# Performance work log

Measured on AMD Instinct MI355X. Metric: run time of the kernel, lower is better.

The kernel has to match this reference:

```python
import jax, jax.numpy as jnp
import numpy as np

EPS = 1e-12  # torch F.normalize eps


def setup_inputs() -> dict:
    key = jax.random.key(0)
    k1, k2, k3 = jax.random.split(key, 3)
    N, C, H, W = 64, 512, 30, 30
    K = 64
    x = jax.random.normal(k1, (N, C, H, W), dtype=jnp.float32)
    conv_w = jax.random.normal(k2, (K, C), dtype=jnp.float32) * 0.02
    centroids = jax.random.uniform(k3, (K, C), dtype=jnp.float32)
    return {"x": x, "conv_w": conv_w, "centroids": centroids}


def reference(x, conv_w, centroids):
    N, C, H, W = x.shape
    K = conv_w.shape[0]
    # descriptor-wise L2 normalization over channel dim (torch F.normalize, p=2, dim=1)
    norm = jnp.sqrt(jnp.sum(x * x, axis=1, keepdims=True))
    x = x / jnp.maximum(norm, EPS)
    xf = x.reshape(N, C, H * W)  # [N, C, P]
    # 1x1 conv (no bias) -> logits [N, K, P]; softmax over clusters K
    logits = jnp.einsum("ncp,kc->nkp", xf, conv_w)
    a = jax.nn.softmax(logits, axis=1)  # [N, K, P]
    # vlad[n,k,c] = sum_p a[n,k,p] * (x[n,c,p] - centroids[k,c])
    #            = (a @ x^T)[n,k,c] - centroids[k,c] * sum_p a[n,k,p]
    vlad = jnp.einsum("nkp,ncp->nkc", a, xf) - a.sum(axis=-1)[:, :, None] * centroids[None]
    return vlad
```

## Files before the change

kernel.cpp:

```cpp
#include <hip/hip_runtime.h>

typedef __attribute__((ext_vector_type(8))) __bf16 bf16x8;
typedef __attribute__((ext_vector_type(4))) __bf16 bf16x4;
typedef __attribute__((ext_vector_type(4))) float f32x4;

#define LGKM_BAR() do { asm volatile("s_waitcnt lgkmcnt(0)" ::: "memory"); \
                        __builtin_amdgcn_s_barrier(); } while (0)

namespace {
constexpr int N_ = 64, C_ = 512, P_ = 900, K_ = 64;
constexpr int PP = 960;
constexpr size_t TOT_X = (size_t)N_ * C_ * P_;
constexpr size_t AT_BYTES = (size_t)N_ * K_ * PP * 2;
constexpr size_t ASUM_OFF = AT_BYTES;
constexpr size_t WBR_OFF  = ASUM_OFF + (size_t)N_ * K_ * 4;
}

__global__ __launch_bounds__(256) void k_prep_w(const float* __restrict__ w,
                                                __bf16* __restrict__ wbr,
                                                float* __restrict__ asum) {
  const int T = blockIdx.x * 256 + threadIdx.x;
  const int k = T >> 6, oct = T & 63;
  const float4 a = *reinterpret_cast<const float4*>(w + (size_t)k * C_ + oct * 8);
  const float4 b = *reinterpret_cast<const float4*>(w + (size_t)k * C_ + oct * 8 + 4);
  bf16x8 o = { (__bf16)a.x, (__bf16)a.y, (__bf16)a.z, (__bf16)a.w,
               (__bf16)b.x, (__bf16)b.y, (__bf16)b.z, (__bf16)b.w };
  *reinterpret_cast<bf16x8*>(wbr + ((size_t)oct * K_ + k) * 8) = o;
  asum[T] = 0.f;
}

__global__ __launch_bounds__(512) void k_phase1(const float* __restrict__ x,
                                                const __bf16* __restrict__ wbr,
                                                __bf16* __restrict__ at,
                                                float* __restrict__ asum) {
  __shared__ bf16x8 Wl[4096];
  const int n   = blockIdx.y;
  const int tid = threadIdx.x;
  const int w   = tid >> 6, l = tid & 63;
  const int l15 = l & 15,  lh = l >> 4;
  const int p   = blockIdx.x * 128 + w * 16 + l15;
  const int pc  = p < P_ ? p : P_ - 1;
  const float* xp = x + (size_t)n * C_ * P_ + (size_t)lh * 8 * P_ + pc;

  bf16x8 tmp[8];
  #pragma unroll
  for (int it = 0; it < 8; ++it)
    tmp[it] = *reinterpret_cast<const bf16x8*>(wbr + (size_t)(it * 512 + tid) * 8);

  float g[6][8];
  #pragma unroll
  for (int b = 0; b < 6; ++b)
    #pragma unroll
    for (int j = 0; j < 8; ++j)
      g[b][j] = xp[(size_t)(b * 32 + j) * P_];

  #pragma unroll
  for (int it = 0; it < 8; ++it)
    Wl[it * 512 + tid] = tmp[it];
  LGKM_BAR();

  f32x4 acc[4] = {};
  float sq = 0.f;
  #pragma unroll
  for (int s = 0; s < 16; ++s) {
    bf16x8 b;
    #pragma unroll
    for (int j = 0; j < 8; ++j) {
      const float v = g[s % 6][j];
      sq = fmaf(v, v, sq); b[j] = (__bf16)v;
    }
    if (s + 6 < 16) {
      #pragma unroll
      for (int j = 0; j < 8; ++j)
        g[s % 6][j] = xp[(size_t)((s + 6) * 32 + j) * P_];
    }
    #pragma unroll
    for (int m = 0; m < 4; ++m) {
      bf16x8 a = Wl[(s * 4 + lh) * 64 + 16 * m + l15];
      acc[m] = __builtin_amdgcn_mfma_f32_16x16x32_bf16(a, b, acc[m], 0, 0, 0);
    }
  }

  sq += __shfl_xor(sq, 16, 64);
  sq += __shfl_xor(sq, 32, 64);
  const float invn = 1.f / fmaxf(sqrtf(sq), 1e-12f);
  const bool  valid = p < P_;

  float ps = 0.f;
  #pragma unroll
  for (int m = 0; m < 4; ++m)
    #pragma unroll
    for (int r = 0; r < 4; ++r) {
      acc[m][r] = __expf(acc[m][r] * invn);
      ps += acc[m][r];
    }
  ps += __shfl_xor(ps, 16, 64);
  ps += __shfl_xor(ps, 32, 64);
  const float invs = 1.f / ps;
  const float sc   = invs * invn;

  if (p < PP) {
    #pragma unroll
    for (int m = 0; m < 4; ++m)
      #pragma unroll
      for (int r = 0; r < 4; ++r) {
        const int k = 16 * m + lh * 4 + r;
        at[((size_t)n * K_ + k) * PP + p] =
            valid ? (__bf16)(acc[m][r] * sc) : (__bf16)0.f;
      }
  }
  #pragma unroll
  for (int m = 0; m < 4; ++m)
    #pragma unroll
    for (int r = 0; r < 4; ++r) {
      float v = valid ? acc[m][r] * invs : 0.f;
      v += __shfl_xor(v, 1, 64); v += __shfl_xor(v, 2, 64);
      v += __shfl_xor(v, 4, 64); v += __shfl_xor(v, 8, 64);
      if (l15 == 0)
        unsafeAtomicAdd(asum + n * K_ + 16 * m + lh * 4 + r, v);
    }
}

__global__ __launch_bounds__(256) void k_phase2(const float* __restrict__ x,
                                                const __bf16* __restrict__ at,
                                                const float* __restrict__ asum,
                                                const float* __restrict__ cent,
                                                float* __restrict__ out) {
  __shared__ __bf16 Al[2][64][40];
  __shared__ __bf16 Xl[2][64][40];
  const int n   = blockIdx.y;
  const int c0  = blockIdx.x * 64;
  const int tid = threadIdx.x;
  const int w   = tid >> 6, l = tid & 63;
  const int l15 = l & 15,  lh = l >> 4;

  const int ak  = tid >> 2, ach = tid & 3;
  const int xc  = tid >> 3, xch = tid & 7;
  const size_t abase  = ((size_t)n * K_ + ak) * PP + ach * 8;
  const size_t xbase0 = ((size_t)n * C_ + c0 + xc) * P_ + xch * 4;
  const size_t xbase1 = ((size_t)n * C_ + c0 + xc + 32) * P_ + xch * 4;

  f32x4 acc[4] = {};
  bf16x8 na; float4 v0, v1;

  auto LOAD = [&](int s) {
    na = *reinterpret_cast<const bf16x8*>(at + abase + s * 32);
    size_t o0 = xbase0 + s * 32; if (o0 > TOT_X - 4) o0 = TOT_X - 4;
    size_t o1 = xbase1 + s * 32; if (o1 > TOT_X - 4) o1 = TOT_X - 4;
    v0 = *reinterpret_cast<const float4*>(x + o0);
    v1 = *reinterpret_cast<const float4*>(x + o1);
  };
  auto STORE = [&](int b) {
    *reinterpret_cast<bf16x8*>(&Al[b][ak][ach * 8]) = na;
    bf16x4 p0 = { (__bf16)v0.x, (__bf16)v0.y, (__bf16)v0.z, (__bf16)v0.w };
    bf16x4 p1 = { (__bf16)v1.x, (__bf16)v1.y, (__bf16)v1.z, (__bf16)v1.w };
    *reinterpret_cast<bf16x4*>(&Xl[b][xc][xch * 4])      = p0;
    *reinterpret_cast<bf16x4*>(&Xl[b][xc + 32][xch * 4]) = p1;
  };

  LOAD(0); STORE(0);
  LGKM_BAR();

  #pragma unroll 2
  for (int s = 0; s < 29; ++s) {
    if (s < 28) LOAD(s + 1);
    bf16x8 b = *reinterpret_cast<const bf16x8*>(&Xl[s & 1][16 * w + l15][lh * 8]);
    #pragma unroll
    for (int m = 0; m < 4; ++m) {
      bf16x8 a = *reinterpret_cast<const bf16x8*>(&Al[s & 1][16 * m + l15][lh * 8]);
      acc[m] = __builtin_amdgcn_mfma_f32_16x16x32_bf16(a, b, acc[m], 0, 0, 0);
    }
    if (s < 28) STORE((s + 1) & 1);
    LGKM_BAR();
  }

  const int c = c0 + 16 * w + l15;
  #pragma unroll
  for (int m = 0; m < 4; ++m) {
    #pragma unroll
    for (int r = 0; r < 4; ++r) {
      const int k = 16 * m + lh * 4 + r;
      out[((size_t)n * K_ + k) * C_ + c] =
          acc[m][r] - asum[n * K_ + k] * cent[(size_t)k * C_ + c];
    }
  }
}

extern "C" void kernel_launch(void* const* d_in, const int* in_sizes, int n_in,
                              void* d_out, int out_size, void* d_ws, size_t ws_size,
                              hipStream_t stream) {
  const float* x    = (const float*)d_in[0];
  const float* w    = (const float*)d_in[1];
  const float* cent = (const float*)d_in[2];
  float* out = (float*)d_out;
  char* wsb  = (char*)d_ws;
  __bf16* at   = (__bf16*)wsb;
  float*  asum = (float*)(wsb + ASUM_OFF);
  __bf16* wbr  = (__bf16*)(wsb + WBR_OFF);

  k_prep_w<<<dim3(16), dim3(256), 0, stream>>>(w, wbr, asum);
  k_phase1<<<dim3(8, 64), dim3(512), 0, stream>>>(x, wbr, at, asum);
  k_phase2<<<dim3(8, 64), dim3(256), 0, stream>>>(x, at, asum, cent, out);
}
```

Measured before the change: 69.82 us.

## Stage phase-1 x tiles through LDS with float4 loads and double buffering

Phase 1 now uses 256-thread blocks covering 64 pixels each (15x64 grid). Previously each lane read x directly with scalar strided loads into registers. Now the block loads coalesced float4 rows into a double-buffered bf16 LDS tile and accumulates per-pixel squared norms through LDS atomics. This should improve global load efficiency and spread work over more blocks. In exchange it adds a barrier per step, strided LDS reads to build the MFMA operand, and a 64 KB weight copy into LDS for every block.

```diff
diff --git a/kernel.cpp b/kernel.cpp
--- a/kernel.cpp
+++ b/kernel.cpp
@@ -29,61 +29,78 @@
   asum[T] = 0.f;
 }
 
-__global__ __launch_bounds__(512) void k_phase1(const float* __restrict__ x,
+__global__ __launch_bounds__(256) void k_phase1(const float* __restrict__ x,
                                                 const __bf16* __restrict__ wbr,
                                                 __bf16* __restrict__ at,
                                                 float* __restrict__ asum) {
   __shared__ bf16x8 Wl[4096];
+  __shared__ __bf16 Xl[2][32][66];
+  __shared__ float ssq_l[64];
   const int n   = blockIdx.y;
+  const int p0  = blockIdx.x * 64;
   const int tid = threadIdx.x;
   const int w   = tid >> 6, l = tid & 63;
   const int l15 = l & 15,  lh = l >> 4;
-  const int p   = blockIdx.x * 128 + w * 16 + l15;
-  const int pc  = p < P_ ? p : P_ - 1;
-  const float* xp = x + (size_t)n * C_ * P_ + (size_t)lh * 8 * P_ + pc;
-
-  bf16x8 tmp[8];
-  #pragma unroll
-  for (int it = 0; it < 8; ++it)
-    tmp[it] = *reinterpret_cast<const bf16x8*>(wbr + (size_t)(it * 512 + tid) * 8);
-
-  float g[6][8];
-  #pragma unroll
-  for (int b = 0; b < 6; ++b)
-    #pragma unroll
-    for (int j = 0; j < 8; ++j)
-      g[b][j] = xp[(size_t)(b * 32 + j) * P_];
-
-  #pragma unroll
-  for (int it = 0; it < 8; ++it)
-    Wl[it * 512 + tid] = tmp[it];
+  const int p   = p0 + w * 16 + l15;
+
+  bf16x8 tmp[16];
+  #pragma unroll
+  for (int it = 0; it < 16; ++it)
+    tmp[it] = *reinterpret_cast<const bf16x8*>(wbr + (size_t)(it * 256 + tid) * 8);
+  #pragma unroll
+  for (int it = 0; it < 16; ++it)
+    Wl[it * 256 + tid] = tmp[it];
+  if (tid < 64) ssq_l[tid] = 0.f;
+
+  const int sc = tid >> 4, pq = (tid & 15) * 4;
+  const bool pvalid = (p0 + pq) < P_;
+  const size_t xs = (size_t)n * C_ * P_ + p0 + pq;
+  float f[8];
+  float sq[4] = {0.f, 0.f, 0.f, 0.f};
+
+  auto LOAD = [&](int s) {
+    if (pvalid) {
+      const float4 v0 = *reinterpret_cast<const float4*>(x + xs + (size_t)(s * 32 + sc) * P_);
+      const float4 v1 = *reinterpret_cast<const float4*>(x + xs + (size_t)(s * 32 + sc + 16) * P_);
+      f[0]=v0.x; f[1]=v0.y; f[2]=v0.z; f[3]=v0.w;
+      f[4]=v1.x; f[5]=v1.y; f[6]=v1.z; f[7]=v1.w;
+    } else {
+      #pragma unroll
+      for (int j = 0; j < 8; ++j) f[j] = 0.f;
+    }
+  };
+  auto STORE = [&](int b) {
+    #pragma unroll
+    for (int j = 0; j < 8; ++j) sq[j & 3] = fmaf(f[j], f[j], sq[j & 3]);
+    bf16x4 a0 = { (__bf16)f[0], (__bf16)f[1], (__bf16)f[2], (__bf16)f[3] };
+    bf16x4 a1 = { (__bf16)f[4], (__bf16)f[5], (__bf16)f[6], (__bf16)f[7] };
+    *reinterpret_cast<bf16x4*>(&Xl[b][sc][pq])      = a0;
+    *reinterpret_cast<bf16x4*>(&Xl[b][sc + 16][pq]) = a1;
+  };
+
+  LOAD(0); STORE(0);
   LGKM_BAR();
 
   f32x4 acc[4] = {};
-  float sq = 0.f;
   #pragma unroll
   for (int s = 0; s < 16; ++s) {
+    if (s < 15) LOAD(s + 1);
     bf16x8 b;
     #pragma unroll
-    for (int j = 0; j < 8; ++j) {
-      const float v = g[s % 6][j];
-      sq = fmaf(v, v, sq); b[j] = (__bf16)v;
-    }
-    if (s + 6 < 16) {
-      #pragma unroll
-      for (int j = 0; j < 8; ++j)
-        g[s % 6][j] = xp[(size_t)((s + 6) * 32 + j) * P_];
-    }
+    for (int j = 0; j < 8; ++j) b[j] = Xl[s & 1][lh * 8 + j][w * 16 + l15];
     #pragma unroll
     for (int m = 0; m < 4; ++m) {
       bf16x8 a = Wl[(s * 4 + lh) * 64 + 16 * m + l15];
       acc[m] = __builtin_amdgcn_mfma_f32_16x16x32_bf16(a, b, acc[m], 0, 0, 0);
     }
+    if (s < 15) { STORE((s + 1) & 1); LGKM_BAR(); }
   }
 
-  sq += __shfl_xor(sq, 16, 64);
-  sq += __shfl_xor(sq, 32, 64);
-  const float invn = 1.f / fmaxf(sqrtf(sq), 1e-12f);
+  #pragma unroll
+  for (int i = 0; i < 4; ++i) atomicAdd(&ssq_l[pq + i], sq[i]);
+  __syncthreads();
+
+  const float invn = 1.f / fmaxf(sqrtf(ssq_l[w * 16 + l15]), 1e-12f);
   const bool  valid = p < P_;
 
   float ps = 0.f;
@@ -97,18 +114,16 @@
   ps += __shfl_xor(ps, 16, 64);
   ps += __shfl_xor(ps, 32, 64);
   const float invs = 1.f / ps;
-  const float sc   = invs * invn;
-
-  if (p < PP) {
-    #pragma unroll
-    for (int m = 0; m < 4; ++m)
-      #pragma unroll
-      for (int r = 0; r < 4; ++r) {
-        const int k = 16 * m + lh * 4 + r;
-        at[((size_t)n * K_ + k) * PP + p] =
-            valid ? (__bf16)(acc[m][r] * sc) : (__bf16)0.f;
-      }
-  }
+  const float sc2  = invs * invn;
+
+  #pragma unroll
+  for (int m = 0; m < 4; ++m)
+    #pragma unroll
+    for (int r = 0; r < 4; ++r) {
+      const int k = 16 * m + lh * 4 + r;
+      at[((size_t)n * K_ + k) * PP + p] =
+          valid ? (__bf16)(acc[m][r] * sc2) : (__bf16)0.f;
+    }
   #pragma unroll
   for (int m = 0; m < 4; ++m)
     #pragma unroll
@@ -199,6 +214,6 @@
   __bf16* wbr  = (__bf16*)(wsb + WBR_OFF);
 
   k_prep_w<<<dim3(16), dim3(256), 0, stream>>>(w, wbr, asum);
-  k_phase1<<<dim3(8, 64), dim3(512), 0, stream>>>(x, wbr, at, asum);
+  k_phase1<<<dim3(15, 64), dim3(256), 0, stream>>>(x, wbr, at, asum);
   k_phase2<<<dim3(8, 64), dim3(256), 0, stream>>>(x, at, asum, cent, out);
 }
```

Result: slower. 83.58 us (+19.7%).

## Stage x through LDS with coalesced float4 loads in phase1, 256 pixels per block

Applied to the files above, without the earlier changes.

Phase1 previously had each lane gather scalar strided x values straight from global memory. It now loads coalesced float4 rows into a double-buffered bf16 LDS tile and accumulates per-pixel squared norms via LDS atomics. Each block covers 256 pixels, with each wave computing two 16-pixel MFMA tiles, so W fragments are reused across both tiles. The grid halves and a launch_bounds occupancy hint is added, in exchange for more LDS use, a barrier per step and padding work on the last block.

```diff
diff --git a/kernel.cpp b/kernel.cpp
--- a/kernel.cpp
+++ b/kernel.cpp
@@ -1,4 +1,5 @@
 #include <hip/hip_runtime.h>
+#include <stdint.h>
 
 typedef __attribute__((ext_vector_type(8))) __bf16 bf16x8;
 typedef __attribute__((ext_vector_type(4))) __bf16 bf16x4;
@@ -10,10 +11,19 @@
 namespace {
 constexpr int N_ = 64, C_ = 512, P_ = 900, K_ = 64;
 constexpr int PP = 960;
+constexpr int PB = 256;
+constexpr int SROW = 266;
 constexpr size_t TOT_X = (size_t)N_ * C_ * P_;
 constexpr size_t AT_BYTES = (size_t)N_ * K_ * PP * 2;
 constexpr size_t ASUM_OFF = AT_BYTES;
 constexpr size_t WBR_OFF  = ASUM_OFF + (size_t)N_ * K_ * 4;
+}
+
+__device__ inline uint32_t pk2(float a, float b) {
+  __bf16 x = (__bf16)a, y = (__bf16)b;
+  uint16_t xb = *reinterpret_cast<uint16_t*>(&x);
+  uint16_t yb = *reinterpret_cast<uint16_t*>(&y);
+  return ((uint32_t)yb << 16) | xb;
 }
 
 __global__ __launch_bounds__(256) void k_prep_w(const float* __restrict__ w,
@@ -29,91 +39,139 @@
   asum[T] = 0.f;
 }
 
-__global__ __launch_bounds__(512) void k_phase1(const float* __restrict__ x,
-                                                const __bf16* __restrict__ wbr,
-                                                __bf16* __restrict__ at,
-                                                float* __restrict__ asum) {
+__global__ __launch_bounds__(512, 2) void k_phase1(const float* __restrict__ x,
+                                                   const __bf16* __restrict__ wbr,
+                                                   __bf16* __restrict__ at,
+                                                   float* __restrict__ asum) {
+  __shared__ __bf16 Xl[2][32][SROW];
   __shared__ bf16x8 Wl[4096];
+  __shared__ float ssq_l[PB];
   const int n   = blockIdx.y;
+  const int p0  = blockIdx.x * PB;
   const int tid = threadIdx.x;
   const int w   = tid >> 6, l = tid & 63;
   const int l15 = l & 15,  lh = l >> 4;
-  const int p   = blockIdx.x * 128 + w * 16 + l15;
-  const int pc  = p < P_ ? p : P_ - 1;
-  const float* xp = x + (size_t)n * C_ * P_ + (size_t)lh * 8 * P_ + pc;
-
-  bf16x8 tmp[8];
+
+  const int sc = tid >> 4;
+  const int pq = (tid & 15) * 16;
+  const float* xrow = x + (size_t)n * C_ * P_ + p0 + pq;
+
+  bf16x8 tw[8];
   #pragma unroll
   for (int it = 0; it < 8; ++it)
-    tmp[it] = *reinterpret_cast<const bf16x8*>(wbr + (size_t)(it * 512 + tid) * 8);
-
-  float g[6][8];
-  #pragma unroll
-  for (int b = 0; b < 6; ++b)
-    #pragma unroll
-    for (int j = 0; j < 8; ++j)
-      g[b][j] = xp[(size_t)(b * 32 + j) * P_];
-
-  #pragma unroll
-  for (int it = 0; it < 8; ++it)
-    Wl[it * 512 + tid] = tmp[it];
+    tw[it] = *reinterpret_cast<const bf16x8*>(wbr + (size_t)(it * 512 + tid) * 8);
+
+  float4 f[2][4];
+  auto LOAD = [&](int s, int slot) {
+    #pragma unroll
+    for (int i = 0; i < 4; ++i) {
+      const int gp = p0 + pq + i * 4;
+      if (gp <= P_ - 4)
+        f[slot][i] = *reinterpret_cast<const float4*>(
+            xrow + (size_t)(s * 32 + sc) * P_ + i * 4);
+      else
+        f[slot][i] = make_float4(0.f, 0.f, 0.f, 0.f);
+    }
+  };
+
+  float sq[16];
+  #pragma unroll
+  for (int j = 0; j < 16; ++j) sq[j] = 0.f;
+
+  auto STORE = [&](int slot, int b) {
+    #pragma unroll
+    for (int i = 0; i < 4; ++i) {
+      const float4 v = f[slot][i];
+      sq[i*4+0] = fmaf(v.x, v.x, sq[i*4+0]);
+      sq[i*4+1] = fmaf(v.y, v.y, sq[i*4+1]);
+      sq[i*4+2] = fmaf(v.z, v.z, sq[i*4+2]);
+      sq[i*4+3] = fmaf(v.w, v.w, sq[i*4+3]);
+      uint32_t* d = reinterpret_cast<uint32_t*>(&Xl[b][sc][pq + i * 4]);
+      d[0] = pk2(v.x, v.y);
+      d[1] = pk2(v.z, v.w);
+    }
+  };
+
+  LOAD(0, 0); LOAD(1, 1);
+  #pragma unroll
+  for (int it = 0; it < 8; ++it) Wl[it * 512 + tid] = tw[it];
+  if (tid < PB) ssq_l[tid] = 0.f;
+  STORE(0, 0);
   LGKM_BAR();
 
-  f32x4 acc[4] = {};
-  float sq = 0.f;
+  f32x4 acc[2][4] = {};
   #pragma unroll
   for (int s = 0; s < 16; ++s) {
-    bf16x8 b;
-    #pragma unroll
-    for (int j = 0; j < 8; ++j) {
-      const float v = g[s % 6][j];
-      sq = fmaf(v, v, sq); b[j] = (__bf16)v;
-    }
-    if (s + 6 < 16) {
+    if (s + 2 < 16) LOAD(s + 2, s & 1);
+    bf16x8 a[4];
+    #pragma unroll
+    for (int m = 0; m < 4; ++m)
+      a[m] = Wl[(s * 4 + lh) * 64 + 16 * m + l15];
+    #pragma unroll
+    for (int t = 0; t < 2; ++t) {
+      bf16x8 bb;
       #pragma unroll
       for (int j = 0; j < 8; ++j)
-        g[s % 6][j] = xp[(size_t)((s + 6) * 32 + j) * P_];
-    }
-    #pragma unroll
-    for (int m = 0; m < 4; ++m) {
-      bf16x8 a = Wl[(s * 4 + lh) * 64 + 16 * m + l15];
-      acc[m] = __builtin_amdgcn_mfma_f32_16x16x32_bf16(a, b, acc[m], 0, 0, 0);
-    }
-  }
-
-  sq += __shfl_xor(sq, 16, 64);
-  sq += __shfl_xor(sq, 32, 64);
-  const float invn = 1.f / fmaxf(sqrtf(sq), 1e-12f);
-  const bool  valid = p < P_;
-
-  float ps = 0.f;
+        bb[j] = Xl[s & 1][lh * 8 + j][w * 32 + t * 16 + l15];
+      #pragma unroll
+      for (int m = 0; m < 4; ++m)
+        acc[t][m] = __builtin_amdgcn_mfma_f32_16x16x32_bf16(a[m], bb, acc[t][m], 0, 0, 0);
+    }
+    if (s < 15) { STORE((s + 1) & 1, (s + 1) & 1); LGKM_BAR(); }
+  }
+
+  #pragma unroll
+  for (int j = 0; j < 16; ++j) atomicAdd(&ssq_l[pq + j], sq[j]);
+  __syncthreads();
+
+  float invn[2], invs[2];
+  bool  val[2];
+  int   pp[2];
+  #pragma unroll
+  for (int t = 0; t < 2; ++t) {
+    pp[t]   = p0 + w * 32 + t * 16 + l15;
+    invn[t] = 1.f / fmaxf(sqrtf(ssq_l[w * 32 + t * 16 + l15]), 1e-12f);
+    val[t]  = pp[t] < P_;
+  }
+  float ps[2] = {0.f, 0.f};
+  #pragma unroll
+  for (int t = 0; t < 2; ++t)
+    #pragma unroll
+    for (int m = 0; m < 4; ++m)
+      #pragma unroll
+      for (int r = 0; r < 4; ++r) {
+        acc[t][m][r] = __expf(acc[t][m][r] * invn[t]);
+        ps[t] += acc[t][m][r];
+      }
+  #pragma unroll
+  for (int t = 0; t < 2; ++t) {
+    ps[t] += __shfl_xor(ps[t], 16, 64);
+    ps[t] += __shfl_xor(ps[t], 32, 64);
+    invs[t] = 1.f / ps[t];
+  }
+
+  #pragma unroll
+  for (int t = 0; t < 2; ++t) {
+    if (pp[t] < PP) {
+      const float sc2 = invs[t] * invn[t];
+      #pragma unroll
+      for (int m = 0; m < 4; ++m)
+        #pragma unroll
+        for (int r = 0; r < 4; ++r) {
+          const int k = 16 * m + lh * 4 + r;
+          at[((size_t)n * K_ + k) * PP + pp[t]] =
+              val[t] ? (__bf16)(acc[t][m][r] * sc2) : (__bf16)0.f;
+        }
+    }
+  }
   #pragma unroll
   for (int m = 0; m < 4; ++m)
     #pragma unroll
     for (int r = 0; r < 4; ++r) {
-      acc[m][r] = __expf(acc[m][r] * invn);
-      ps += acc[m][r];
-    }
-  ps += __shfl_xor(ps, 16, 64);
-  ps += __shfl_xor(ps, 32, 64);
-  const float invs = 1.f / ps;
-  const float sc   = invs * invn;
-
-  if (p < PP) {
-    #pragma unroll
-    for (int m = 0; m < 4; ++m)
-      #pragma unroll
-      for (int r = 0; r < 4; ++r) {
-        const int k = 16 * m + lh * 4 + r;
-        at[((size_t)n * K_ + k) * PP + p] =
-            valid ? (__bf16)(acc[m][r] * sc) : (__bf16)0.f;
-      }
-  }
-  #pragma unroll
-  for (int m = 0; m < 4; ++m)
-    #pragma unroll
-    for (int r = 0; r < 4; ++r) {
-      float v = valid ? acc[m][r] * invs : 0.f;
+      float v = 0.f;
+      #pragma unroll
+      for (int t = 0; t < 2; ++t)
+        v += val[t] ? acc[t][m][r] * invs[t] : 0.f;
       v += __shfl_xor(v, 1, 64); v += __shfl_xor(v, 2, 64);
       v += __shfl_xor(v, 4, 64); v += __shfl_xor(v, 8, 64);
       if (l15 == 0)
@@ -199,6 +257,6 @@
   __bf16* wbr  = (__bf16*)(wsb + WBR_OFF);
 
   k_prep_w<<<dim3(16), dim3(256), 0, stream>>>(w, wbr, asum);
-  k_phase1<<<dim3(8, 64), dim3(512), 0, stream>>>(x, wbr, at, asum);
+  k_phase1<<<dim3(4, 64), dim3(512), 0, stream>>>(x, wbr, at, asum);
   k_phase2<<<dim3(8, 64), dim3(256), 0, stream>>>(x, at, asum, cent, out);
 }
```

Result: slower. 99.03 us (+41.8%).

## Split phase1 into channel-quarter logit partials plus separate softmax kernel

Applied to the files above, without the earlier changes.

Phase1 now has each block stage a 128-channel quarter of one image through LDS with coalesced float4 loads. It writes partial bf16 logits and partial squared norms per quarter. A new softmax kernel sums the four partials, applies normalization, softmax and the cluster sums, then writes the assignment matrix. This replaces strided per-pixel column loads with coalesced ones, at the cost of an extra launch, extra workspace traffic for the partials, and bf16 rounding of the partial logits.

```diff
diff --git a/kernel.cpp b/kernel.cpp
--- a/kernel.cpp
+++ b/kernel.cpp
@@ -1,4 +1,5 @@
 #include <hip/hip_runtime.h>
+#include <stdint.h>
 
 typedef __attribute__((ext_vector_type(8))) __bf16 bf16x8;
 typedef __attribute__((ext_vector_type(4))) __bf16 bf16x4;
@@ -10,10 +11,13 @@
 namespace {
 constexpr int N_ = 64, C_ = 512, P_ = 900, K_ = 64;
 constexpr int PP = 960;
+constexpr int XROW = 962;
 constexpr size_t TOT_X = (size_t)N_ * C_ * P_;
 constexpr size_t AT_BYTES = (size_t)N_ * K_ * PP * 2;
 constexpr size_t ASUM_OFF = AT_BYTES;
 constexpr size_t WBR_OFF  = ASUM_OFF + (size_t)N_ * K_ * 4;
+constexpr size_t SSQ_OFF  = WBR_OFF + (size_t)K_ * C_ * 2;
+constexpr size_t LQ_OFF   = SSQ_OFF + (size_t)4 * N_ * PP * 4;
 }
 
 __global__ __launch_bounds__(256) void k_prep_w(const float* __restrict__ w,
@@ -31,94 +35,171 @@
 
 __global__ __launch_bounds__(512) void k_phase1(const float* __restrict__ x,
                                                 const __bf16* __restrict__ wbr,
-                                                __bf16* __restrict__ at,
-                                                float* __restrict__ asum) {
-  __shared__ bf16x8 Wl[4096];
-  const int n   = blockIdx.y;
+                                                __bf16* __restrict__ Lq,
+                                                float* __restrict__ ssqq) {
+  __shared__ __bf16 Xa[2][32][XROW];
+  __shared__ bf16x8 Wl[1024];
+  const int bid = blockIdx.x;
+  const int n = bid >> 2, q = bid & 3;
   const int tid = threadIdx.x;
-  const int w   = tid >> 6, l = tid & 63;
-  const int l15 = l & 15,  lh = l >> 4;
-  const int p   = blockIdx.x * 128 + w * 16 + l15;
-  const int pc  = p < P_ ? p : P_ - 1;
-  const float* xp = x + (size_t)n * C_ * P_ + (size_t)lh * 8 * P_ + pc;
-
-  bf16x8 tmp[8];
-  #pragma unroll
-  for (int it = 0; it < 8; ++it)
-    tmp[it] = *reinterpret_cast<const bf16x8*>(wbr + (size_t)(it * 512 + tid) * 8);
-
-  float g[6][8];
-  #pragma unroll
-  for (int b = 0; b < 6; ++b)
-    #pragma unroll
-    for (int j = 0; j < 8; ++j)
-      g[b][j] = xp[(size_t)(b * 32 + j) * P_];
-
-  #pragma unroll
-  for (int it = 0; it < 8; ++it)
-    Wl[it * 512 + tid] = tmp[it];
+  const int w = tid >> 6, l = tid & 63;
+  const int l15 = l & 15, lh = l >> 4;
+  const int wk = w >> 2, wp = w & 3;
+
+  {
+    const bf16x8* wq = reinterpret_cast<const bf16x8*>(wbr) + (size_t)q * 1024;
+    bf16x8 t0 = wq[tid], t1 = wq[512 + tid];
+    Wl[tid] = t0; Wl[512 + tid] = t1;
+  }
+  for (int idx = tid; idx < 2 * 32 * 62; idx += 512) {
+    const int b = idx / 1984, r = idx - b * 1984;
+    Xa[b][r / 62][900 + r % 62] = (__bf16)0.f;
+  }
+
+  const float* xbase = x + ((size_t)n * C_ + q * 128) * P_;
+  float4 ring[15];
+  const bool stg = tid < 480;
+
+  auto LOADS = [&](int s) {
+    if (stg) {
+      #pragma unroll
+      for (int i = 0; i < 15; ++i)
+        ring[i] = *reinterpret_cast<const float4*>(
+            xbase + (size_t)s * 28800 + (size_t)(tid + i * 480) * 4);
+    }
+  };
+  auto STORES = [&](int buf) {
+    if (stg) {
+      #pragma unroll
+      for (int i = 0; i < 15; ++i) {
+        const int fo = tid + i * 480;
+        const int c = fo / 225, pq4 = (fo - c * 225) * 4;
+        const float4 v = ring[i];
+        bf16x4 o = { (__bf16)v.x, (__bf16)v.y, (__bf16)v.z, (__bf16)v.w };
+        *reinterpret_cast<bf16x4*>(&Xa[buf][c][pq4]) = o;
+      }
+    }
+  };
+
+  LOADS(0); STORES(0);
   LGKM_BAR();
 
-  f32x4 acc[4] = {};
-  float sq = 0.f;
-  #pragma unroll
-  for (int s = 0; s < 16; ++s) {
-    bf16x8 b;
-    #pragma unroll
-    for (int j = 0; j < 8; ++j) {
-      const float v = g[s % 6][j];
-      sq = fmaf(v, v, sq); b[j] = (__bf16)v;
-    }
-    if (s + 6 < 16) {
-      #pragma unroll
-      for (int j = 0; j < 8; ++j)
-        g[s % 6][j] = xp[(size_t)((s + 6) * 32 + j) * P_];
-    }
-    #pragma unroll
-    for (int m = 0; m < 4; ++m) {
-      bf16x8 a = Wl[(s * 4 + lh) * 64 + 16 * m + l15];
-      acc[m] = __builtin_amdgcn_mfma_f32_16x16x32_bf16(a, b, acc[m], 0, 0, 0);
-    }
-  }
-
-  sq += __shfl_xor(sq, 16, 64);
-  sq += __shfl_xor(sq, 32, 64);
-  const float invn = 1.f / fmaxf(sqrtf(sq), 1e-12f);
-  const bool  valid = p < P_;
-
-  float ps = 0.f;
-  #pragma unroll
-  for (int m = 0; m < 4; ++m)
-    #pragma unroll
-    for (int r = 0; r < 4; ++r) {
-      acc[m][r] = __expf(acc[m][r] * invn);
-      ps += acc[m][r];
-    }
-  ps += __shfl_xor(ps, 16, 64);
-  ps += __shfl_xor(ps, 32, 64);
-  const float invs = 1.f / ps;
-  const float sc   = invs * invn;
-
-  if (p < PP) {
-    #pragma unroll
-    for (int m = 0; m < 4; ++m)
+  f32x4 acc[15][2] = {};
+  float sq0 = 0.f, sq1 = 0.f;
+  const int p1c = 512 + tid;
+
+  #pragma unroll
+  for (int s = 0; s < 4; ++s) {
+    if (s < 3) LOADS(s + 1);
+    const int buf = s & 1;
+    #pragma unroll
+    for (int t = 0; t < 15; ++t) {
+      const int p = wp * 240 + t * 16 + l15;
+      bf16x8 b;
+      #pragma unroll
+      for (int j = 0; j < 8; ++j) b[j] = Xa[buf][lh * 8 + j][p];
+      #pragma unroll
+      for (int m = 0; m < 2; ++m) {
+        bf16x8 a = Wl[(s * 4 + lh) * 64 + wk * 32 + m * 16 + l15];
+        acc[t][m] = __builtin_amdgcn_mfma_f32_16x16x32_bf16(a, b, acc[t][m], 0, 0, 0);
+      }
+    }
+    #pragma unroll
+    for (int cc = 0; cc < 32; ++cc) {
+      const float v0 = (float)Xa[buf][cc][tid];
+      sq0 = fmaf(v0, v0, sq0);
+      if (p1c < PP) { const float v1 = (float)Xa[buf][cc][p1c]; sq1 = fmaf(v1, v1, sq1); }
+    }
+    if (s < 3) { STORES((s + 1) & 1); LGKM_BAR(); }
+  }
+
+  float* sqo = ssqq + ((size_t)q * N_ + n) * PP;
+  sqo[tid] = sq0;
+  if (p1c < PP) sqo[p1c] = sq1;
+
+  __bf16* lqo = Lq + ((size_t)q * N_ + n) * K_ * PP;
+  #pragma unroll
+  for (int t = 0; t < 15; ++t) {
+    const int p = wp * 240 + t * 16 + l15;
+    #pragma unroll
+    for (int m = 0; m < 2; ++m)
       #pragma unroll
       for (int r = 0; r < 4; ++r) {
-        const int k = 16 * m + lh * 4 + r;
-        at[((size_t)n * K_ + k) * PP + p] =
-            valid ? (__bf16)(acc[m][r] * sc) : (__bf16)0.f;
+        const int k = wk * 32 + m * 16 + lh * 4 + r;
+        lqo[(size_t)k * PP + p] = (__bf16)acc[t][m][r];
       }
   }
-  #pragma unroll
-  for (int m = 0; m < 4; ++m)
-    #pragma unroll
-    for (int r = 0; r < 4; ++r) {
-      float v = valid ? acc[m][r] * invs : 0.f;
-      v += __shfl_xor(v, 1, 64); v += __shfl_xor(v, 2, 64);
-      v += __shfl_xor(v, 4, 64); v += __shfl_xor(v, 8, 64);
-      if (l15 == 0)
-        unsafeAtomicAdd(asum + n * K_ + 16 * m + lh * 4 + r, v);
-    }
+}
+
+__global__ __launch_bounds__(256) void k_softmax(const __bf16* __restrict__ Lq,
+                                                 const float* __restrict__ ssqq,
+                                                 __bf16* __restrict__ at,
+                                                 float* __restrict__ asum) {
+  __shared__ float invn_l[64], invs_l[64], S_l[64], ak_l[64];
+  __shared__ float Ls[64][66];
+  const int n = blockIdx.y, pt = blockIdx.x;
+  const int t = threadIdx.x;
+  const int k = t & 63, pg = t >> 6;
+
+  if (t < 64) {
+    float ss = 0.f;
+    #pragma unroll
+    for (int q2 = 0; q2 < 4; ++q2)
+      ss += ssqq[((size_t)q2 * N_ + n) * PP + pt * 64 + t];
+    invn_l[t] = 1.f / fmaxf(sqrtf(ss), 1e-12f);
+    S_l[t] = 0.f; ak_l[t] = 0.f;
+  }
+  __syncthreads();
+
+  float L[16];
+  #pragma unroll
+  for (int i = 0; i < 16; ++i) L[i] = 0.f;
+  const size_t QS = (size_t)N_ * K_ * PP;
+  const __bf16* lb = Lq + ((size_t)n * K_ + k) * PP + pt * 64 + pg * 16;
+  #pragma unroll
+  for (int q2 = 0; q2 < 4; ++q2) {
+    bf16x8 u0 = *reinterpret_cast<const bf16x8*>(lb + q2 * QS);
+    bf16x8 u1 = *reinterpret_cast<const bf16x8*>(lb + q2 * QS + 8);
+    #pragma unroll
+    for (int i = 0; i < 8; ++i) { L[i] += (float)u0[i]; L[8 + i] += (float)u1[i]; }
+  }
+  float e[16];
+  #pragma unroll
+  for (int i = 0; i < 16; ++i) {
+    const int p = pt * 64 + pg * 16 + i;
+    e[i] = (p < P_) ? __expf(L[i] * invn_l[pg * 16 + i]) : 0.f;
+    Ls[k][pg * 16 + i] = e[i];
+  }
+  __syncthreads();
+  {
+    const int pl = t & 63, kc = t >> 6;
+    float s = 0.f;
+    #pragma unroll
+    for (int kk = 0; kk < 16; ++kk) s += Ls[kc * 16 + kk][pl];
+    atomicAdd(&S_l[pl], s);
+  }
+  __syncthreads();
+  if (t < 64) {
+    const float S = S_l[t];
+    invs_l[t] = (S > 0.f) ? 1.f / S : 0.f;
+  }
+  __syncthreads();
+
+  float aps = 0.f;
+  bf16x8 o0, o1;
+  #pragma unroll
+  for (int i = 0; i < 16; ++i) {
+    const float a = e[i] * invs_l[pg * 16 + i];
+    aps += a;
+    const float ap = a * invn_l[pg * 16 + i];
+    if (i < 8) o0[i] = (__bf16)ap; else o1[i - 8] = (__bf16)ap;
+  }
+  __bf16* ao = at + ((size_t)n * K_ + k) * PP + pt * 64 + pg * 16;
+  *reinterpret_cast<bf16x8*>(ao)     = o0;
+  *reinterpret_cast<bf16x8*>(ao + 8) = o1;
+  atomicAdd(&ak_l[k], aps);
+  __syncthreads();
+  if (t < 64) unsafeAtomicAdd(asum + n * K_ + t, ak_l[t]);
 }
 
 __global__ __launch_bounds__(256) void k_phase2(const float* __restrict__ x,
@@ -197,8 +278,11 @@
   __bf16* at   = (__bf16*)wsb;
   float*  asum = (float*)(wsb + ASUM_OFF);
   __bf16* wbr  = (__bf16*)(wsb + WBR_OFF);
+  float*  ssqq = (float*)(wsb + SSQ_OFF);
+  __bf16* Lq   = (__bf16*)(wsb + LQ_OFF);
 
   k_prep_w<<<dim3(16), dim3(256), 0, stream>>>(w, wbr, asum);
-  k_phase1<<<dim3(8, 64), dim3(512), 0, stream>>>(x, wbr, at, asum);
+  k_phase1<<<dim3(256), dim3(512), 0, stream>>>(x, wbr, Lq, ssqq);
+  k_softmax<<<dim3(15, 64), dim3(256), 0, stream>>>(Lq, ssqq, at, asum);
   k_phase2<<<dim3(8, 64), dim3(256), 0, stream>>>(x, at, asum, cent, out);
 }
```

Result: slower. 140.7 us (+101.5%).
